# Optimization experiments

Hardware: AMD Instinct MI355X
Metric: run time of the kernel (lower is better)

## Reference

```python
import jax, jax.numpy as jnp
import numpy as np

EMBED, HEADS, LEVELS, POINTS = 256, 8, 1, 4


def setup_inputs():
    key = jax.random.key(0)
    ks = jax.random.split(key, 8)
    B, NQ = 8, 8192
    Hh, Ww = 128, 128
    E, Hn, L, P = EMBED, HEADS, LEVELS, POINTS
    s = 1.0 / np.sqrt(E)
    return dict(
        query=jax.random.normal(ks[0], (B, NQ, E), jnp.float32),
        value=jax.random.normal(ks[1], (B, Hh * Ww, E), jnp.float32),
        ref_2d=jax.random.uniform(ks[2], (B, NQ, L, 2), dtype=jnp.float32),
        spatial_shapes=jnp.array([[Hh, Ww]], dtype=jnp.int32),
        W_off=jax.random.normal(ks[3], (E, Hn * L * P * 2), jnp.float32) * 0.01,
        b_off=jax.random.normal(ks[4], (Hn * L * P * 2,), jnp.float32) * 0.5,
        W_attn=jax.random.normal(ks[5], (E, Hn * L * P), jnp.float32) * s,
        b_attn=jnp.zeros((Hn * L * P,), jnp.float32),
        W_val=jax.random.normal(ks[6], (E, E), jnp.float32) * s,
        b_val=jnp.zeros((E,), jnp.float32),
        W_out=jax.random.normal(ks[7], (E, E), jnp.float32) * s,
        b_out=jnp.zeros((E,), jnp.float32),
    )


def _bilinear_sample(v, loc, Hl, Wl):
    # v: (B, Hn, Hl*Wl, dh); loc: (B, Hn, NQ, P, 2) normalized [0,1] (x, y)
    B, Hn, NQ, P, _ = loc.shape
    dh = v.shape[-1]
    # torch grid_sample(align_corners=False) pixel coords: p = loc * size - 0.5
    x = loc[..., 0] * Wl - 0.5
    y = loc[..., 1] * Hl - 0.5
    x0 = jnp.floor(x); y0 = jnp.floor(y)
    x1 = x0 + 1.0; y1 = y0 + 1.0
    wx1 = x - x0; wx0 = 1.0 - wx1
    wy1 = y - y0; wy0 = 1.0 - wy1

    def corner(xc, yc, w):
        valid = (xc >= 0) & (xc < Wl) & (yc >= 0) & (yc < Hl)  # zeros padding
        xi = jnp.clip(xc, 0, Wl - 1).astype(jnp.int32)
        yi = jnp.clip(yc, 0, Hl - 1).astype(jnp.int32)
        idx = (yi * Wl + xi).reshape(B, Hn, NQ * P, 1)
        vals = jnp.take_along_axis(v, idx, axis=2).reshape(B, Hn, NQ, P, dh)
        return vals * (w * valid.astype(v.dtype))[..., None]

    return (corner(x0, y0, wx0 * wy0) + corner(x1, y0, wx1 * wy0)
            + corner(x0, y1, wx0 * wy1) + corner(x1, y1, wx1 * wy1))


def _forward(query, value, ref_2d, W_off, b_off, W_attn, b_attn, W_val, b_val, W_out, b_out, shapes):
    B, NQ, E = query.shape
    Hn, L, P = HEADS, LEVELS, POINTS
    dh = E // Hn
    NV = value.shape[1]
    identity = query
    v = (value @ W_val + b_val).reshape(B, NV, Hn, dh)
    off = (query @ W_off + b_off).reshape(B, NQ, Hn, L, P, 2)
    attn = jax.nn.softmax((query @ W_attn + b_attn).reshape(B, NQ, Hn, L * P), axis=-1)
    attn = attn.reshape(B, NQ, Hn, L, P)
    # offset_normalizer = (W, H) per level
    norm = jnp.asarray(shapes[:, ::-1].copy(), dtype=query.dtype)
    loc = ref_2d[:, :, None, :, None, :] + off / norm[None, None, None, :, None, :]
    loc = jnp.transpose(loc, (0, 2, 1, 3, 4, 5))   # (B, Hn, NQ, L, P, 2)
    attn_t = jnp.transpose(attn, (0, 2, 1, 3, 4))  # (B, Hn, NQ, L, P)
    v_t = jnp.transpose(v, (0, 2, 1, 3))           # (B, Hn, NV, dh)
    starts = np.concatenate([[0], np.cumsum(shapes[:, 0] * shapes[:, 1])]).astype(np.int64)
    out = jnp.zeros((B, Hn, NQ, dh), query.dtype)
    for l in range(L):  # static small loop over feature levels
        Hl, Wl = int(shapes[l, 0]), int(shapes[l, 1])
        v_l = v_t[:, :, int(starts[l]):int(starts[l + 1]), :]
        samp = _bilinear_sample(v_l, loc[:, :, :, l], Hl, Wl)  # (B,Hn,NQ,P,dh)
        out = out + jnp.sum(samp * attn_t[:, :, :, l, :, None], axis=3)
    out = jnp.transpose(out, (0, 2, 1, 3)).reshape(B, NQ, E)
    # dropout is identity at eval time
    return out @ W_out + b_out + identity


def reference(query, value, ref_2d, spatial_shapes, W_off, b_off, W_attn, b_attn, W_val, b_val, W_out, b_out):
    shapes = np.asarray(jax.device_get(spatial_shapes))  # static level shapes
    return _forward(query, value, ref_2d, W_off, b_off, W_attn, b_attn, W_val, b_val, W_out, b_out, shapes)
```

## Files before the change

### kernel.cpp

```cpp
#include <hip/hip_runtime.h>

typedef short s16x8 __attribute__((ext_vector_type(8)));
typedef float f32x4 __attribute__((ext_vector_type(4)));

#define HN 8
#define PP 4
#define DH 32
#define NQc 8192
#define NVc 16384
#define EE 256
#define HWc 128

__device__ __forceinline__ unsigned short f2bf(float x) {
  unsigned u = __float_as_uint(x);
  u += 0x7FFF + ((u >> 16) & 1);
  return (unsigned short)(u >> 16);
}
__device__ __forceinline__ float bf2f(unsigned short h) {
  return __uint_as_float(((unsigned)h) << 16);
}
__device__ __forceinline__ unsigned cvt2(float lo, float hi) {
  unsigned r;
  asm("v_cvt_pk_bf16_f32 %0, %1, %2" : "=v"(r) : "v"(lo), "v"(hi));
  return r;
}
__device__ __forceinline__ void gld16(const void* g, void* l) {
  __builtin_amdgcn_global_load_lds(
      (const __attribute__((address_space(1))) void*)g,
      (__attribute__((address_space(3))) void*)l, 16, 0, 0);
}

__global__ __launch_bounds__(256) void wprep(
    const float* __restrict__ Wval, const float* __restrict__ Wout,
    const float* __restrict__ Woff, const float* __restrict__ Wattn,
    const float* __restrict__ boff, const float* __restrict__ battn,
    unsigned short* __restrict__ wvt, unsigned short* __restrict__ wot,
    unsigned short* __restrict__ wct, float* __restrict__ bcat) {
  int g = blockIdx.x * 256 + threadIdx.x;
  if (g < 65536) {
    int n = g >> 8, k = g & 255;
    wvt[n * 256 + k] = f2bf(Wval[k * 256 + n]);
  } else if (g < 131072) {
    int g2 = g - 65536;
    int n = g2 >> 8, k = g2 & 255;
    wot[n * 256 + k] = f2bf(Wout[k * 256 + n]);
  } else if (g < 163840) {
    int g2 = g - 131072;
    int n = g2 >> 8, k = g2 & 255;
    float v = 0.f;
    if (n < 64) v = Woff[k * 64 + n];
    else if (n < 96) v = Wattn[k * 32 + (n - 64)];
    wct[n * 256 + k] = f2bf(v);
  } else if (g < 163968) {
    int c = g - 163840;
    bcat[c] = (c < 64) ? boff[c] : ((c < 96) ? battn[c - 64] : 0.f);
  }
}

#define MODE_VAL 0
#define MODE_PLAIN 1
#define MODE_OUT 2

template <int MODE>
struct SmemBytes { static constexpr int v = 49152; };
template <> struct SmemBytes<MODE_PLAIN> { static constexpr int v = 51200; };
template <> struct SmemBytes<MODE_OUT>   { static constexpr int v = 33792; };

template <int MODE, bool ABF16>
__global__ __launch_bounds__(256) void mfma_gemm(
    const void* __restrict__ Ain, const unsigned short* __restrict__ Wt,
    const float* __restrict__ bias, const float* __restrict__ resid,
    const float* __restrict__ ref2d, unsigned int* __restrict__ meta,
    void* __restrict__ outp) {
  __shared__ __align__(16) char smem[SmemBytes<MODE>::v];
  constexpr int ATILE = ABF16 ? 8192 : 16384;
  char* A0 = smem;
  char* A1 = smem + ATILE;
  unsigned short* W0 = (unsigned short*)(smem + 2 * ATILE);
  unsigned short* W1 = W0 + 4096;

  const int t = threadIdx.x;
  const int lane = t & 63, wave = t >> 6;
  const int lane15 = lane & 15, quad = lane >> 4;
  const int wr = wave >> 1, wc = wave & 1;
  const int bm = blockIdx.x * 128, bn = blockIdx.y * 128;

  f32x4 acc[4][4];
#pragma unroll
  for (int i = 0; i < 4; ++i)
#pragma unroll
    for (int j = 0; j < 4; ++j)
#pragma unroll
      for (int r = 0; r < 4; ++r) acc[i][j][r] = 0.f;

  const unsigned short* Wtb = Wt + (size_t)bn * 256;
#define ISSUE_W(K0, WD)                                                        \
  do {                                                                         \
    _Pragma("unroll") for (int i = 0; i < 2; ++i) {                            \
      const int ii = wave * 2 + i;                                             \
      const int row = ii * 16 + (lane >> 2);                                   \
      const int slot = (lane & 3) ^ ((lane >> 2) & 3);                         \
      gld16(Wtb + (size_t)row * 256 + (K0) + slot * 8, (WD) + ii * 512);       \
    }                                                                          \
  } while (0)
#define ISSUE_A(K0, AD)                                                        \
  do {                                                                         \
    if (!ABF16) {                                                              \
      const float* Af = (const float*)Ain + (size_t)bm * 256;                  \
      _Pragma("unroll") for (int i = 0; i < 4; ++i) {                          \
        const int ii = wave * 4 + i;                                           \
        const int row = ii * 8 + (lane >> 3);                                  \
        const int slot = (lane & 7) ^ (lane >> 3);                             \
        gld16(Af + (size_t)row * 256 + (K0) + slot * 4, (AD) + ii * 1024);     \
      }                                                                        \
    } else {                                                                   \
      const unsigned short* Ab = (const unsigned short*)Ain + (size_t)bm * 256;\
      _Pragma("unroll") for (int i = 0; i < 2; ++i) {                          \
        const int ii = wave * 2 + i;                                           \
        const int row = ii * 16 + (lane >> 2);                                 \
        const int slot = (lane & 3) ^ ((lane >> 2) & 3);                       \
        gld16(Ab + (size_t)row * 256 + (K0) + slot * 8, (AD) + ii * 1024);     \
      }                                                                        \
    }                                                                          \
  } while (0)

  ISSUE_A(0, A0);
  ISSUE_W(0, W0);

#pragma unroll
  for (int kk = 0; kk < 8; ++kk) {
    __syncthreads();
    if (kk < 7) {
      if (kk & 1) { ISSUE_A((kk + 1) * 32, A0); ISSUE_W((kk + 1) * 32, W0); }
      else        { ISSUE_A((kk + 1) * 32, A1); ISSUE_W((kk + 1) * 32, W1); }
    }
    const char* Ar = (kk & 1) ? A1 : A0;
    const unsigned short* Wr = (kk & 1) ? W1 : W0;

    s16x8 af[4], bfr[4];
#pragma unroll
    for (int tm = 0; tm < 4; ++tm) {
      const int row = wr * 64 + tm * 16 + lane15;
      if (!ABF16) {
        const float* Arf = (const float*)Ar;
        const int r7 = lane15 & 7;
        const f32x4 x0 = *(const f32x4*)&Arf[row * 32 + (((quad * 2)     ^ r7) * 4)];
        const f32x4 x1 = *(const f32x4*)&Arf[row * 32 + (((quad * 2 + 1) ^ r7) * 4)];
        union { unsigned u[4]; s16x8 v; } tu;
        tu.u[0] = cvt2(x0[0], x0[1]); tu.u[1] = cvt2(x0[2], x0[3]);
        tu.u[2] = cvt2(x1[0], x1[1]); tu.u[3] = cvt2(x1[2], x1[3]);
        af[tm] = tu.v;
      } else {
        const unsigned short* Arb = (const unsigned short*)Ar;
        const int r3 = lane15 & 3;
        af[tm] = *(const s16x8*)&Arb[row * 32 + ((quad ^ r3) * 8)];
      }
    }
#pragma unroll
    for (int tn = 0; tn < 4; ++tn) {
      const int row = wc * 64 + tn * 16 + lane15;
      const int r3 = lane15 & 3;
      bfr[tn] = *(const s16x8*)&Wr[row * 32 + ((quad ^ r3) * 8)];
    }
#pragma unroll
    for (int tm = 0; tm < 4; ++tm)
#pragma unroll
      for (int tn = 0; tn < 4; ++tn)
        acc[tm][tn] = __builtin_amdgcn_mfma_f32_16x16x32_bf16(bfr[tn], af[tm], acc[tm][tn], 0, 0, 0);
  }
#undef ISSUE_A
#undef ISSUE_W

  if (MODE == MODE_VAL) {
    unsigned short* outs = (unsigned short*)outp;
    const size_t b = (size_t)(bm >> 14);
    const int n0 = bm & (NVc - 1);
#pragma unroll
    for (int tn = 0; tn < 4; ++tn) {
      const int ch0 = bn + wc * 64 + tn * 16 + quad * 4;
      const float4 b4 = *(const float4*)&bias[ch0];
      const int h = ch0 >> 5, dh0 = ch0 & 31;
#pragma unroll
      for (int tm = 0; tm < 4; ++tm) {
        const int n = n0 + wr * 64 + tm * 16 + lane15;
        ushort4 o;
        o.x = f2bf(acc[tm][tn][0] + b4.x);
        o.y = f2bf(acc[tm][tn][1] + b4.y);
        o.z = f2bf(acc[tm][tn][2] + b4.z);
        o.w = f2bf(acc[tm][tn][3] + b4.w);
        *(ushort4*)(outs + ((b * HN + h) * NVc + n) * DH + dh0) = o;
      }
    }
  } else if (MODE == MODE_PLAIN) {
    float* Cf = (float*)smem;
    __syncthreads();
#pragma unroll
    for (int tn = 0; tn < 4; ++tn) {
      const int col0 = wc * 64 + tn * 16 + quad * 4;
      if (col0 < 96) {
        const float4 b4 = *(const float4*)&bias[col0];
#pragma unroll
        for (int tm = 0; tm < 4; ++tm) {
          const int m = wr * 64 + tm * 16 + lane15;
          float4 v;
          v.x = acc[tm][tn][0] + b4.x;
          v.y = acc[tm][tn][1] + b4.y;
          v.z = acc[tm][tn][2] + b4.z;
          v.w = acc[tm][tn][3] + b4.w;
          *(float4*)&Cf[m * 100 + col0] = v;
        }
      }
    }
    __syncthreads();
#pragma unroll
    for (int i = 0; i < 4; ++i) {
      const int task = i * 256 + t;
      const int h = task & 7, rowl = task >> 3;
      const int bq = bm + rowl;
      const float* row = Cf + rowl * 100;
      const float rx = ref2d[(size_t)bq * 2 + 0];
      const float ry = ref2d[(size_t)bq * 2 + 1];
      const float l0 = row[64 + h * 4 + 0], l1 = row[64 + h * 4 + 1];
      const float l2 = row[64 + h * 4 + 2], l3 = row[64 + h * 4 + 3];
      const float mx = fmaxf(fmaxf(l0, l1), fmaxf(l2, l3));
      float e0 = __expf(l0 - mx), e1 = __expf(l1 - mx), e2 = __expf(l2 - mx), e3 = __expf(l3 - mx);
      const float inv = 1.0f / (e0 + e1 + e2 + e3);
      float ee[4] = {e0, e1, e2, e3};
      unsigned int* m = meta + ((size_t)bq * 8 + h) * 20;
      uint4 pk;
      float4 wts[4];
#pragma unroll
      for (int p = 0; p < PP; ++p) {
        const float a = ee[p] * inv;
        const float ox = row[h * 8 + p * 2 + 0];
        const float oy = row[h * 8 + p * 2 + 1];
        const float x = (rx + ox * (1.0f / HWc)) * (float)HWc - 0.5f;
        const float y = (ry + oy * (1.0f / HWc)) * (float)HWc - 0.5f;
        const float x0f = floorf(x), y0f = floorf(y);
        const int x0 = (int)x0f, y0 = (int)y0f;
        const float wx1 = x - x0f, wx0 = 1.f - wx1;
        const float wy1 = y - y0f, wy0 = 1.f - wy1;
        const bool vx0 = (unsigned)x0 < (unsigned)HWc, vx1 = (unsigned)(x0 + 1) < (unsigned)HWc;
        const bool vy0 = (unsigned)y0 < (unsigned)HWc, vy1 = (unsigned)(y0 + 1) < (unsigned)HWc;
        const int xi0 = min(max(x0, 0), HWc - 1), xi1 = min(max(x0 + 1, 0), HWc - 1);
        const int yi0 = min(max(y0, 0), HWc - 1), yi1 = min(max(y0 + 1, 0), HWc - 1);
        const unsigned pv = (unsigned)xi0 | ((unsigned)yi0 << 8) | ((unsigned)xi1 << 16) | ((unsigned)yi1 << 24);
        if (p == 0) pk.x = pv; else if (p == 1) pk.y = pv; else if (p == 2) pk.z = pv; else pk.w = pv;
        float4 w;
        w.x = (vx0 && vy0) ? a * wx0 * wy0 : 0.f;
        w.y = (vx1 && vy0) ? a * wx1 * wy0 : 0.f;
        w.z = (vx0 && vy1) ? a * wx0 * wy1 : 0.f;
        w.w = (vx1 && vy1) ? a * wx1 * wy1 : 0.f;
        wts[p] = w;
      }
      *(uint4*)m = pk;
#pragma unroll
      for (int p = 0; p < PP; ++p) *(float4*)&m[4 + p * 4] = wts[p];
    }
  } else {
    float* Cf = (float*)smem;
    float* outf = (float*)outp;
#pragma unroll
    for (int pass = 0; pass < 2; ++pass) {
      __syncthreads();
      if (wr == pass) {
#pragma unroll
        for (int tn = 0; tn < 4; ++tn) {
          const int col0 = wc * 64 + tn * 16 + quad * 4;
          const float4 b4 = *(const float4*)&bias[bn + col0];
#pragma unroll
          for (int tm = 0; tm < 4; ++tm) {
            const int rowl = tm * 16 + lane15;
            float4 v;
            v.x = acc[tm][tn][0] + b4.x;
            v.y = acc[tm][tn][1] + b4.y;
            v.z = acc[tm][tn][2] + b4.z;
            v.w = acc[tm][tn][3] + b4.w;
            *(float4*)&Cf[rowl * 132 + col0] = v;
          }
        }
      }
      __syncthreads();
#pragma unroll
      for (int i = 0; i < 8; ++i) {
        const int id = i * 256 + t;
        const int n = id >> 5, c = id & 31;
        const size_t row = (size_t)bm + pass * 64 + n;
        float4 v = *(const float4*)&Cf[n * 132 + c * 4];
        float4 rs = *(const float4*)(resid + row * 256 + bn + c * 4);
        v.x += rs.x; v.y += rs.y; v.z += rs.z; v.w += rs.w;
        *(float4*)(outf + row * 256 + bn + c * 4) = v;
      }
    }
  }
}

__global__ __launch_bounds__(256) void sample_kernel(
    const unsigned short* __restrict__ vbuf,
    const unsigned int* __restrict__ meta,
    unsigned short* __restrict__ outs) {
  const int t = threadIdx.x;
  const int d4 = (t & 7) << 2;
  const int ql = t >> 3;
  const int sl = blockIdx.x >> 8;
  const int qc = blockIdx.x & 255;
  const int b = sl >> 3;
  const int h = sl & 7;
  const int q = qc * 32 + ql;
  const size_t bq = (size_t)b * NQc + q;
  const unsigned int* m = meta + ((size_t)bq * 8 + h) * 20;
  const uint4 pk = *(const uint4*)m;
  const unsigned short* vb = vbuf + (size_t)sl * (NVc * DH) + d4;

  float4 acc = {0.f, 0.f, 0.f, 0.f};
#pragma unroll
  for (int p = 0; p < PP; ++p) {
    const unsigned P = (p == 0) ? pk.x : (p == 1) ? pk.y : (p == 2) ? pk.z : pk.w;
    const float4 w = *(const float4*)(m + 4 + p * 4);
    const int x0 = P & 255, y0 = (P >> 8) & 255, x1 = (P >> 16) & 255, y1 = P >> 24;
    const int r0 = y0 << 12, r1 = y1 << 12;
    const ushort4 v00 = *(const ushort4*)(vb + r0 + (x0 << 5));
    const ushort4 v10 = *(const ushort4*)(vb + r0 + (x1 << 5));
    const ushort4 v01 = *(const ushort4*)(vb + r1 + (x0 << 5));
    const ushort4 v11 = *(const ushort4*)(vb + r1 + (x1 << 5));
    acc.x += w.x * bf2f(v00.x); acc.y += w.x * bf2f(v00.y);
    acc.z += w.x * bf2f(v00.z); acc.w += w.x * bf2f(v00.w);
    acc.x += w.y * bf2f(v10.x); acc.y += w.y * bf2f(v10.y);
    acc.z += w.y * bf2f(v10.z); acc.w += w.y * bf2f(v10.w);
    acc.x += w.z * bf2f(v01.x); acc.y += w.z * bf2f(v01.y);
    acc.z += w.z * bf2f(v01.z); acc.w += w.z * bf2f(v01.w);
    acc.x += w.w * bf2f(v11.x); acc.y += w.w * bf2f(v11.y);
    acc.z += w.w * bf2f(v11.z); acc.w += w.w * bf2f(v11.w);
  }
  ushort4 o;
  o.x = f2bf(acc.x); o.y = f2bf(acc.y); o.z = f2bf(acc.z); o.w = f2bf(acc.w);
  *(ushort4*)(outs + bq * EE + h * DH + d4) = o;
}

extern "C" void kernel_launch(void* const* d_in, const int* in_sizes, int n_in,
                              void* d_out, int out_size, void* d_ws, size_t ws_size,
                              hipStream_t stream) {
  const float* query = (const float*)d_in[0];
  const float* value = (const float*)d_in[1];
  const float* ref2d = (const float*)d_in[2];
  const float* Woff  = (const float*)d_in[4];
  const float* boff  = (const float*)d_in[5];
  const float* Wattn = (const float*)d_in[6];
  const float* battn = (const float*)d_in[7];
  const float* Wval  = (const float*)d_in[8];
  const float* bval  = (const float*)d_in[9];
  const float* Wout  = (const float*)d_in[10];
  const float* bout  = (const float*)d_in[11];
  float* out = (float*)d_out;

  unsigned short* vbuf = (unsigned short*)d_ws;
  unsigned int* meta   = (unsigned int*)(vbuf + 33554432);
  unsigned short* sbuf = (unsigned short*)(meta + 10485760);
  unsigned short* wvt  = sbuf + 16777216;
  unsigned short* wot  = wvt + 65536;
  unsigned short* wct  = wot + 65536;
  float* bcat          = (float*)(wct + 32768);

  wprep<<<641, 256, 0, stream>>>(Wval, Wout, Woff, Wattn, boff, battn, wvt, wot, wct, bcat);

  mfma_gemm<MODE_VAL, false><<<dim3(1024, 2), 256, 0, stream>>>(
      (const void*)value, wvt, bval, nullptr, nullptr, nullptr, (void*)vbuf);

  mfma_gemm<MODE_PLAIN, false><<<dim3(512, 1), 256, 0, stream>>>(
      (const void*)query, wct, bcat, nullptr, ref2d, meta, nullptr);

  sample_kernel<<<16384, 256, 0, stream>>>(vbuf, meta, sbuf);

  mfma_gemm<MODE_OUT, true><<<dim3(512, 2), 256, 0, stream>>>(
      (const void*)sbuf, wot, bout, query, nullptr, nullptr, (void*)out);
}
```

Baseline: 422.6 us.

## Load GEMM operands directly from global memory instead of LDS staging

Removes the double-buffered global-to-LDS staging (global_load_lds plus barriers) and has each lane load its MFMA fragments straight from global memory. The grid is also transposed so blocks sharing the same A rows are launched next to each other, which should improve cache reuse of the A tile across the N blocks. This drops barrier and LDS traffic but loses the explicit prefetch overlap, and the fragment loads become strided per-lane reads that now depend on L1/L2 for reuse. The barrier before the PLAIN epilogue's LDS write is also removed, which is safe only because the main loop no longer uses LDS.

Result: slower. 486.4 us (+15.1%).

```diff
diff --git a/kernel.cpp b/kernel.cpp
--- a/kernel.cpp
+++ b/kernel.cpp
@@ -23,11 +23,6 @@
   unsigned r;
   asm("v_cvt_pk_bf16_f32 %0, %1, %2" : "=v"(r) : "v"(lo), "v"(hi));
   return r;
-}
-__device__ __forceinline__ void gld16(const void* g, void* l) {
-  __builtin_amdgcn_global_load_lds(
-      (const __attribute__((address_space(1))) void*)g,
-      (__attribute__((address_space(3))) void*)l, 16, 0, 0);
 }
 
 __global__ __launch_bounds__(256) void wprep(
@@ -62,7 +57,7 @@
 #define MODE_OUT 2
 
 template <int MODE>
-struct SmemBytes { static constexpr int v = 49152; };
+struct SmemBytes { static constexpr int v = 16; };
 template <> struct SmemBytes<MODE_PLAIN> { static constexpr int v = 51200; };
 template <> struct SmemBytes<MODE_OUT>   { static constexpr int v = 33792; };
 
@@ -73,17 +68,11 @@
     const float* __restrict__ ref2d, unsigned int* __restrict__ meta,
     void* __restrict__ outp) {
   __shared__ __align__(16) char smem[SmemBytes<MODE>::v];
-  constexpr int ATILE = ABF16 ? 8192 : 16384;
-  char* A0 = smem;
-  char* A1 = smem + ATILE;
-  unsigned short* W0 = (unsigned short*)(smem + 2 * ATILE);
-  unsigned short* W1 = W0 + 4096;
-
   const int t = threadIdx.x;
   const int lane = t & 63, wave = t >> 6;
   const int lane15 = lane & 15, quad = lane >> 4;
   const int wr = wave >> 1, wc = wave & 1;
-  const int bm = blockIdx.x * 128, bn = blockIdx.y * 128;
+  const int bn = blockIdx.x * 128, bm = blockIdx.y * 128;
 
   f32x4 acc[4][4];
 #pragma unroll
@@ -93,83 +82,38 @@
 #pragma unroll
       for (int r = 0; r < 4; ++r) acc[i][j][r] = 0.f;
 
-  const unsigned short* Wtb = Wt + (size_t)bn * 256;
-#define ISSUE_W(K0, WD)                                                        \
-  do {                                                                         \
-    _Pragma("unroll") for (int i = 0; i < 2; ++i) {                            \
-      const int ii = wave * 2 + i;                                             \
-      const int row = ii * 16 + (lane >> 2);                                   \
-      const int slot = (lane & 3) ^ ((lane >> 2) & 3);                         \
-      gld16(Wtb + (size_t)row * 256 + (K0) + slot * 8, (WD) + ii * 512);       \
-    }                                                                          \
-  } while (0)
-#define ISSUE_A(K0, AD)                                                        \
-  do {                                                                         \
-    if (!ABF16) {                                                              \
-      const float* Af = (const float*)Ain + (size_t)bm * 256;                  \
-      _Pragma("unroll") for (int i = 0; i < 4; ++i) {                          \
-        const int ii = wave * 4 + i;                                           \
-        const int row = ii * 8 + (lane >> 3);                                  \
-        const int slot = (lane & 7) ^ (lane >> 3);                             \
-        gld16(Af + (size_t)row * 256 + (K0) + slot * 4, (AD) + ii * 1024);     \
-      }                                                                        \
-    } else {                                                                   \
-      const unsigned short* Ab = (const unsigned short*)Ain + (size_t)bm * 256;\
-      _Pragma("unroll") for (int i = 0; i < 2; ++i) {                          \
-        const int ii = wave * 2 + i;                                           \
-        const int row = ii * 16 + (lane >> 2);                                 \
-        const int slot = (lane & 3) ^ ((lane >> 2) & 3);                       \
-        gld16(Ab + (size_t)row * 256 + (K0) + slot * 8, (AD) + ii * 1024);     \
-      }                                                                        \
-    }                                                                          \
-  } while (0)
-
-  ISSUE_A(0, A0);
-  ISSUE_W(0, W0);
+  const int arow = bm + wr * 64 + lane15;
+  const int wrow = bn + wc * 64 + lane15;
+  const float* Af = (const float*)Ain;
+  const unsigned short* Ab = (const unsigned short*)Ain;
 
 #pragma unroll
   for (int kk = 0; kk < 8; ++kk) {
-    __syncthreads();
-    if (kk < 7) {
-      if (kk & 1) { ISSUE_A((kk + 1) * 32, A0); ISSUE_W((kk + 1) * 32, W0); }
-      else        { ISSUE_A((kk + 1) * 32, A1); ISSUE_W((kk + 1) * 32, W1); }
-    }
-    const char* Ar = (kk & 1) ? A1 : A0;
-    const unsigned short* Wr = (kk & 1) ? W1 : W0;
-
+    const int k0 = kk * 32;
     s16x8 af[4], bfr[4];
 #pragma unroll
     for (int tm = 0; tm < 4; ++tm) {
-      const int row = wr * 64 + tm * 16 + lane15;
       if (!ABF16) {
-        const float* Arf = (const float*)Ar;
-        const int r7 = lane15 & 7;
-        const f32x4 x0 = *(const f32x4*)&Arf[row * 32 + (((quad * 2)     ^ r7) * 4)];
-        const f32x4 x1 = *(const f32x4*)&Arf[row * 32 + (((quad * 2 + 1) ^ r7) * 4)];
+        const float* p = Af + (size_t)(arow + tm * 16) * 256 + k0 + quad * 8;
+        const float4 x0 = *(const float4*)p;
+        const float4 x1 = *(const float4*)(p + 4);
         union { unsigned u[4]; s16x8 v; } tu;
-        tu.u[0] = cvt2(x0[0], x0[1]); tu.u[1] = cvt2(x0[2], x0[3]);
-        tu.u[2] = cvt2(x1[0], x1[1]); tu.u[3] = cvt2(x1[2], x1[3]);
+        tu.u[0] = cvt2(x0.x, x0.y); tu.u[1] = cvt2(x0.z, x0.w);
+        tu.u[2] = cvt2(x1.x, x1.y); tu.u[3] = cvt2(x1.z, x1.w);
         af[tm] = tu.v;
       } else {
-        const unsigned short* Arb = (const unsigned short*)Ar;
-        const int r3 = lane15 & 3;
-        af[tm] = *(const s16x8*)&Arb[row * 32 + ((quad ^ r3) * 8)];
-      }
-    }
-#pragma unroll
-    for (int tn = 0; tn < 4; ++tn) {
-      const int row = wc * 64 + tn * 16 + lane15;
-      const int r3 = lane15 & 3;
-      bfr[tn] = *(const s16x8*)&Wr[row * 32 + ((quad ^ r3) * 8)];
-    }
+        af[tm] = *(const s16x8*)(Ab + (size_t)(arow + tm * 16) * 256 + k0 + quad * 8);
+      }
+    }
+#pragma unroll
+    for (int tn = 0; tn < 4; ++tn)
+      bfr[tn] = *(const s16x8*)(Wt + (size_t)(wrow + tn * 16) * 256 + k0 + quad * 8);
 #pragma unroll
     for (int tm = 0; tm < 4; ++tm)
 #pragma unroll
       for (int tn = 0; tn < 4; ++tn)
         acc[tm][tn] = __builtin_amdgcn_mfma_f32_16x16x32_bf16(bfr[tn], af[tm], acc[tm][tn], 0, 0, 0);
   }
-#undef ISSUE_A
-#undef ISSUE_W
 
   if (MODE == MODE_VAL) {
     unsigned short* outs = (unsigned short*)outp;
@@ -193,7 +137,6 @@
     }
   } else if (MODE == MODE_PLAIN) {
     float* Cf = (float*)smem;
-    __syncthreads();
 #pragma unroll
     for (int tn = 0; tn < 4; ++tn) {
       const int col0 = wc * 64 + tn * 16 + quad * 4;
@@ -363,14 +306,14 @@
 
   wprep<<<641, 256, 0, stream>>>(Wval, Wout, Woff, Wattn, boff, battn, wvt, wot, wct, bcat);
 
-  mfma_gemm<MODE_VAL, false><<<dim3(1024, 2), 256, 0, stream>>>(
+  mfma_gemm<MODE_VAL, false><<<dim3(2, 1024), 256, 0, stream>>>(
       (const void*)value, wvt, bval, nullptr, nullptr, nullptr, (void*)vbuf);
 
-  mfma_gemm<MODE_PLAIN, false><<<dim3(512, 1), 256, 0, stream>>>(
+  mfma_gemm<MODE_PLAIN, false><<<dim3(1, 512), 256, 0, stream>>>(
       (const void*)query, wct, bcat, nullptr, ref2d, meta, nullptr);
 
   sample_kernel<<<16384, 256, 0, stream>>>(vbuf, meta, sbuf);
 
-  mfma_gemm<MODE_OUT, true><<<dim3(512, 2), 256, 0, stream>>>(
+  mfma_gemm<MODE_OUT, true><<<dim3(2, 512), 256, 0, stream>>>(
       (const void*)sbuf, wot, bout, query, nullptr, nullptr, (void*)out);
 }
```
